# Performance work log

Hardware: AMD Instinct MI355X
Metric: run time of the kernel (lower is better)

## Reference

```python
import jax, jax.numpy as jnp
import numpy as np

B, Nq, C = 1, 40000, 256
Hh, L, P = 8, 4, 8
hd = C // Hh
LEVEL_SHAPES = [(128, 128), (64, 64), (32, 32), (16, 16)]


def setup_inputs() -> dict:
    key = jax.random.key(0)
    ks = jax.random.split(key, 16)
    inp = {}
    inp['query'] = jax.random.normal(ks[0], (B, Nq, C), jnp.float32)
    # reference points in [-1, 1] normalized coords (x, y)
    inp['reference_points'] = jax.random.uniform(ks[1], (B, Nq, L, 2), jnp.float32) * 2.0 - 1.0
    for i, (h, w) in enumerate(LEVEL_SHAPES):
        inp[f'feat{i}'] = jax.random.normal(ks[2 + i], (B, C, h, w), jnp.float32)
    # learned params (torch Linear y = x @ W + b, W stored as [in, out])
    inp['W_off'] = jax.random.normal(ks[6], (C, Hh * L * P * 2), jnp.float32) * 0.02
    inp['b_off'] = jax.random.normal(ks[7], (Hh * L * P * 2,), jnp.float32) * 0.5
    inp['W_attn'] = jax.random.normal(ks[8], (C, Hh * L * P), jnp.float32) * 0.02
    inp['b_attn'] = jnp.zeros((Hh * L * P,), jnp.float32)
    inp['W_val'] = jax.random.normal(ks[9], (C, C), jnp.float32) * (1.0 / np.sqrt(C))
    inp['b_val'] = jnp.zeros((C,), jnp.float32)
    inp['W_out'] = jax.random.normal(ks[10], (C, C), jnp.float32) * (1.0 / np.sqrt(C))
    inp['b_out'] = jnp.zeros((C,), jnp.float32)
    return inp


def _deform_sample(v, coords):
    # Bilinear grid_sample, align_corners=True, zeros padding.
    # v: [B, Hh, H, W, hd]; coords: [B, Hh, S, 2] in [-1, 1] (x, y)
    _, _, H, W, _ = v.shape
    x = (coords[..., 0] + 1.0) * 0.5 * (W - 1)
    y = (coords[..., 1] + 1.0) * 0.5 * (H - 1)
    x0 = jnp.floor(x)
    y0 = jnp.floor(y)
    vflat = v.reshape(v.shape[0], v.shape[1], H * W, v.shape[4])

    def corner(xi, yi, w):
        inb = (xi >= 0) & (xi <= W - 1) & (yi >= 0) & (yi <= H - 1)
        idx = (jnp.clip(yi, 0, H - 1) * W + jnp.clip(xi, 0, W - 1)).astype(jnp.int32)
        g = jnp.take_along_axis(vflat, idx[..., None], axis=2)  # [B,Hh,S,hd]
        return g * (w * inb)[..., None]

    return (corner(x0, y0, (x0 + 1 - x) * (y0 + 1 - y))
            + corner(x0 + 1, y0, (x - x0) * (y0 + 1 - y))
            + corner(x0, y0 + 1, (x0 + 1 - x) * (y - y0))
            + corner(x0 + 1, y0 + 1, (x - x0) * (y - y0)))


def reference(query, feat0, feat1, feat2, feat3, reference_points,
              W_off, b_off, W_attn, b_attn, W_val, b_val, W_out, b_out):
    feats = [feat0, feat1, feat2, feat3]
    off = (query @ W_off + b_off).reshape(B, Nq, Hh, L, P, 2)
    w = (query @ W_attn + b_attn).reshape(B, Nq, Hh, L, P)
    w = jax.nn.softmax(w, axis=-1)  # softmax over points, per level
    # samp: [B, Nq, Hh, L, P, 2]
    samp = reference_points[:, :, None, :, None, :] + jnp.tanh(off) * 0.25

    out = jnp.zeros((B, Nq, Hh, hd), jnp.float32)
    for l, f in enumerate(feats):
        Hl, Wl = f.shape[2], f.shape[3]
        v = jnp.einsum('bchw,cd->bhwd', f, W_val) + b_val  # value proj
        v = v.reshape(B, Hl, Wl, Hh, hd).transpose(0, 3, 1, 2, 4)  # [B,Hh,H,W,hd]
        coords = samp[:, :, :, l].transpose(0, 2, 1, 3, 4).reshape(B, Hh, Nq * P, 2)
        s = _deform_sample(v, coords).reshape(B, Hh, Nq, P, hd)
        wl = w[:, :, :, l].transpose(0, 2, 1, 3)  # [B,Hh,Nq,P]
        out = out + jnp.einsum('bhnpd,bhnp->bnhd', s, wl)

    return out.reshape(B, Nq, C) @ W_out + b_out
```

## Files before the change

### kernel.cpp

```cpp
#include <hip/hip_runtime.h>
#include <hip/hip_fp16.h>
#include <math.h>

#define NQ 40000

typedef short s16x8 __attribute__((ext_vector_type(8)));
typedef float f32x4 __attribute__((ext_vector_type(4)));

static constexpr int HLa[4] = {128, 64, 32, 16};
static constexpr int HWa[4] = {16384, 4096, 1024, 256};
static constexpr int VB[4] = {0, 4194304, 5242880, 5505024};

__device__ __forceinline__ short bf16hi(float x) {
    union { float f; unsigned u; } v; v.f = x;
    unsigned r = v.u + 0x7FFFu + ((v.u >> 16) & 1u);
    return (short)(r >> 16);
}
__device__ __forceinline__ float bf16f(short s) {
    union { unsigned u; float f; } v; v.u = ((unsigned)(unsigned short)s) << 16;
    return v.f;
}
__device__ __forceinline__ float fast_tanh(float x) {
    float xc = fminf(fmaxf(x, -15.f), 15.f);
    float e = __expf(2.f * xc);
    return (e - 1.f) / (e + 1.f);
}
#define MFMA16(a, b, c) __builtin_amdgcn_mfma_f32_16x16x32_bf16(a, b, c, 0, 0, 0)

__global__ __launch_bounds__(256) void prep_w(
    const float* __restrict__ Woff, const float* __restrict__ Wattn,
    const float* __restrict__ Wout, short* __restrict__ WtH, short* __restrict__ WtL)
{
    int r = blockIdx.x, c = threadIdx.x;
    float x;
    if (r < 512)      x = Woff[c * 512 + r];
    else if (r < 768) x = Wattn[c * 256 + (r - 512)];
    else              x = Wout[c * 256 + (r - 768)];
    short hi = bf16hi(x);
    WtH[r * 256 + c] = hi;
    WtL[r * 256 + c] = bf16hi(x - bf16f(hi));
}

__global__ __launch_bounds__(256) void vproj_kernel(
    const float* __restrict__ f0, const float* __restrict__ f1,
    const float* __restrict__ f2, const float* __restrict__ f3,
    const float* __restrict__ Wv, const float* __restrict__ bv,
    __half* __restrict__ v)
{
    __shared__ float fT[256 * 16];

    int bid = blockIdx.x;
    const float* f;
    int base, HWl, hw0;
    if (bid < 1024)      { f = f0; base = VB[0]; HWl = 16384; hw0 = bid * 16; }
    else if (bid < 1280) { f = f1; base = VB[1]; HWl = 4096;  hw0 = (bid - 1024) * 16; }
    else if (bid < 1344) { f = f2; base = VB[2]; HWl = 1024;  hw0 = (bid - 1280) * 16; }
    else                 { f = f3; base = VB[3]; HWl = 256;   hw0 = (bid - 1344) * 16; }

    int t = threadIdx.x;
    for (int k = 0; k < 16; ++k) {
        int idx = k * 256 + t;
        int c = idx >> 4, j = idx & 15;
        fT[idx] = f[c * HWl + hw0 + j];
    }
    __syncthreads();

    int to4 = (t & 63) * 4;
    int hw4 = (t >> 6) * 4;

    float4 bv4 = *(const float4*)(bv + to4);
    float acc[4][4];
    #pragma unroll
    for (int i = 0; i < 4; ++i) {
        acc[i][0] = bv4.x; acc[i][1] = bv4.y; acc[i][2] = bv4.z; acc[i][3] = bv4.w;
    }

    #pragma unroll 4
    for (int c = 0; c < 256; ++c) {
        float4 w4 = *(const float4*)(Wv + c * 256 + to4);
        float4 fv = *(const float4*)(fT + c * 16 + hw4);
        float fa[4] = {fv.x, fv.y, fv.z, fv.w};
        float wa[4] = {w4.x, w4.y, w4.z, w4.w};
        #pragma unroll
        for (int i = 0; i < 4; ++i)
            #pragma unroll
            for (int j = 0; j < 4; ++j)
                acc[i][j] += fa[i] * wa[j];
    }

    int hh = to4 >> 5, dd4 = to4 & 31;
    #pragma unroll
    for (int i = 0; i < 4; ++i) {
        int hw = hw0 + hw4 + i;
        __half2 h0 = __floats2half2_rn(acc[i][0], acc[i][1]);
        __half2 h1 = __floats2half2_rn(acc[i][2], acc[i][3]);
        uint2 st = make_uint2(*(unsigned*)&h0, *(unsigned*)&h1);
        *(uint2*)(v + base + (hh * HWl + hw) * 32 + dd4) = st;
    }
}

__global__ __launch_bounds__(256, 4) void msda_kernel(
    const float* __restrict__ query, const float* __restrict__ refp,
    const float* __restrict__ boff,  const float* __restrict__ battn,
    const float* __restrict__ bout,
    const short* __restrict__ WtH,   const short* __restrict__ WtL,
    const __half* __restrict__ v,    float* __restrict__ out)
{
    __shared__ __align__(16) char lds[37888];
    short*    sQh  = (short*)lds;
    short*    sQl  = (short*)(lds + 8448);
    float*    offL = (float*)lds;
    uint2*    sPWh = (uint2*)(lds + 8448);
    float*    sWf  = (float*)(lds + 16896);
    unsigned* sPI  = (unsigned*)(lds + 33280);
    float*    sR   = (float*)(lds + 37376);

    const int t = threadIdx.x;
    const int n0 = blockIdx.x * 16;
    const int wv = t >> 6, lane = t & 63;
    const int mrow = lane & 15, kg = lane >> 4;

    for (int k2 = 0; k2 < 16; ++k2) {
        float x = query[(n0 + k2) * 256 + t];
        short hi = bf16hi(x);
        sQh[k2 * 264 + t] = hi;
        sQl[k2 * 264 + t] = bf16hi(x - bf16f(hi));
    }
    if (t < 128) sR[t] = refp[n0 * 8 + t];
    __syncthreads();

    f32x4 accO[8], accA[4];
    {
        f32x4 z = {0.f, 0.f, 0.f, 0.f};
        #pragma unroll
        for (int j = 0; j < 8; ++j) accO[j] = z;
        #pragma unroll
        for (int j = 0; j < 4; ++j) accA[j] = z;
    }
    {
        const short* offH = WtH + (wv * 128 + mrow) * 256 + kg * 8;
        const short* offLo = WtL + (wv * 128 + mrow) * 256 + kg * 8;
        const short* attH = WtH + (512 + wv * 64 + mrow) * 256 + kg * 8;
        const short* attL = WtL + (512 + wv * 64 + mrow) * 256 + kg * 8;
        const int aoff = mrow * 264 + kg * 8;
        #pragma unroll
        for (int kk = 0; kk < 8; ++kk) {
            s16x8 ah = *(const s16x8*)(sQh + aoff + kk * 32);
            s16x8 al = *(const s16x8*)(sQl + aoff + kk * 32);
            #pragma unroll
            for (int j = 0; j < 8; ++j) {
                s16x8 bh = *(const s16x8*)(offH + j * 4096 + kk * 32);
                s16x8 bl = *(const s16x8*)(offLo + j * 4096 + kk * 32);
                accO[j] = MFMA16(ah, bh, accO[j]);
                accO[j] = MFMA16(al, bh, accO[j]);
                accO[j] = MFMA16(ah, bl, accO[j]);
            }
            #pragma unroll
            for (int ja = 0; ja < 4; ++ja) {
                s16x8 bh = *(const s16x8*)(attH + ja * 4096 + kk * 32);
                s16x8 bl = *(const s16x8*)(attL + ja * 4096 + kk * 32);
                accA[ja] = MFMA16(ah, bh, accA[ja]);
                accA[ja] = MFMA16(al, bh, accA[ja]);
                accA[ja] = MFMA16(ah, bl, accA[ja]);
            }
        }
    }
    #pragma unroll
    for (int j = 0; j < 8; ++j) {
        float bb = boff[wv * 128 + j * 16 + mrow];
        #pragma unroll
        for (int r = 0; r < 4; ++r) accO[j][r] += bb;
    }
    #pragma unroll
    for (int ja = 0; ja < 4; ++ja) {
        float bb = battn[wv * 64 + ja * 16 + mrow];
        #pragma unroll
        for (int r = 0; r < 4; ++r) accA[ja][r] += bb;
    }

    #pragma unroll
    for (int ja = 0; ja < 4; ++ja) {
        int hh = 2 * wv + (ja >> 1);
        int l  = ((ja & 1) << 1) | (mrow >> 3);
        int p  = mrow & 7;
        #pragma unroll
        for (int r = 0; r < 4; ++r) {
            float x = accA[ja][r];
            float m = fmaxf(x, __shfl_xor(x, 1));
            m = fmaxf(m, __shfl_xor(m, 2));
            m = fmaxf(m, __shfl_xor(m, 4));
            float e = __expf(x - m);
            float s = e + __shfl_xor(e, 1);
            s += __shfl_xor(s, 2);
            s += __shfl_xor(s, 4);
            int q = kg * 4 + r;
            sWf[q * 256 + hh * 32 + l * 8 + p] = e / s;
        }
    }
    __syncthreads();

    const int dd2 = t & 15, hhpS = (t >> 4) & 1, qp = t >> 5;

    for (int k = 0; k < 4; ++k) {
        if (wv == k) {
            #pragma unroll
            for (int j = 0; j < 8; ++j)
                #pragma unroll
                for (int r = 0; r < 4; ++r)
                    offL[(kg * 4 + r) * 132 + j * 16 + mrow] = accO[j][r];
        }
        __syncthreads();

        #pragma unroll
        for (int it = 0; it < 4; ++it) {
            int s = it * 256 + t;
            int q = s >> 6, hhL = (s >> 5) & 1, l = (s >> 3) & 3, p = s & 7;
            const int Wl = 128 >> l;
            const float scl = 0.5f * (float)(Wl - 1);
            float lx = offL[q * 132 + hhL * 64 + l * 16 + p * 2];
            float ly = offL[q * 132 + hhL * 64 + l * 16 + p * 2 + 1];
            float w  = sWf[q * 256 + (2 * k + hhL) * 32 + l * 8 + p];
            float rx = sR[q * 8 + l * 2], ry = sR[q * 8 + l * 2 + 1];
            float cx = rx + fast_tanh(lx) * 0.25f;
            float cy = ry + fast_tanh(ly) * 0.25f;
            float xx = (cx + 1.f) * scl, yy = (cy + 1.f) * scl;
            float x0f = floorf(xx), y0f = floorf(yy);
            float fx = xx - x0f, fy = yy - y0f;
            int x0 = (int)x0f, y0 = (int)y0f;
            int xc0 = min(max(x0, 0), Wl - 1);
            int xc1 = min(max(x0 + 1, 0), Wl - 1);
            int yc0 = min(max(y0, 0), Wl - 1);
            int yc1 = min(max(y0 + 1, 0), Wl - 1);
            bool bx0 = (x0 >= 0) & (x0 < Wl);
            bool bx1 = (x0 + 1 >= 0) & (x0 + 1 < Wl);
            bool by0 = (y0 >= 0) & (y0 < Wl);
            bool by1 = (y0 + 1 >= 0) & (y0 + 1 < Wl);
            float w00 = (bx0 && by0) ? (1.f - fx) * (1.f - fy) * w : 0.f;
            float w01 = (bx1 && by0) ? fx * (1.f - fy) * w : 0.f;
            float w10 = (bx0 && by1) ? (1.f - fx) * fy * w : 0.f;
            float w11 = (bx1 && by1) ? fx * fy * w : 0.f;
            unsigned pw = (unsigned)(yc0 * Wl + xc0)
                        | ((unsigned)(xc1 - xc0) << 14)
                        | ((unsigned)(yc1 - yc0) << 15);
            sPI[s] = pw;
            __half2 hA = __floats2half2_rn(w00, w01);
            __half2 hB = __floats2half2_rn(w10, w11);
            sPWh[s] = make_uint2(*(unsigned*)&hA, *(unsigned*)&hB);
        }
        __syncthreads();

        {
            const int hh = 2 * k + hhpS;
            #pragma unroll
            for (int qi2 = 0; qi2 < 2; ++qi2) {
                int qi = qp * 2 + qi2;
                float accx = 0.f, accy = 0.f;
                #pragma unroll
                for (int l = 0; l < 4; ++l) {
                    const int Wl = HLa[l];
                    const __half2* vl = (const __half2*)(v + VB[l] + hh * HWa[l] * 32 + dd2 * 2);
                    int sbase = ((qi * 2 + hhpS) * 4 + l) * 8;
                    #pragma unroll
                    for (int p = 0; p < 8; ++p) {
                        unsigned pw = sPI[sbase + p];
                        uint2 ww = sPWh[sbase + p];
                        float2 fa = __half22float2(*(__half2*)&ww.x);
                        float2 fb = __half22float2(*(__half2*)&ww.y);
                        int idx = pw & 0x3FFF;
                        int dxo = ((pw >> 14) & 1) * 16;
                        int dyo = ((pw >> 15) & 1) * (Wl * 16);
                        const __half2* b00 = vl + idx * 16;
                        float2 f00 = __half22float2(b00[0]);
                        float2 f01 = __half22float2(b00[dxo]);
                        float2 f10 = __half22float2(b00[dyo]);
                        float2 f11 = __half22float2(b00[dxo + dyo]);
                        accx += fa.x * f00.x + fa.y * f01.x + fb.x * f10.x + fb.y * f11.x;
                        accy += fa.x * f00.y + fa.y * f01.y + fb.x * f10.y + fb.y * f11.y;
                    }
                }
                *(float2*)(sWf + qi * 256 + hh * 32 + dd2 * 2) = make_float2(accx, accy);
            }
        }
        __syncthreads();
    }

    {
        int q = t >> 4, c0 = (t & 15) * 16;
        #pragma unroll
        for (int j = 0; j < 16; ++j) {
            float x = sWf[q * 256 + c0 + j];
            short hi = bf16hi(x);
            sQh[q * 264 + c0 + j] = hi;
            sQl[q * 264 + c0 + j] = bf16hi(x - bf16f(hi));
        }
    }
    __syncthreads();

    {
        f32x4 accE[4];
        f32x4 z = {0.f, 0.f, 0.f, 0.f};
        #pragma unroll
        for (int e = 0; e < 4; ++e) accE[e] = z;
        const short* outH = WtH + (768 + wv * 64 + mrow) * 256 + kg * 8;
        const short* outL = WtL + (768 + wv * 64 + mrow) * 256 + kg * 8;
        const int aoff = mrow * 264 + kg * 8;
        #pragma unroll
        for (int kk = 0; kk < 8; ++kk) {
            s16x8 ah = *(const s16x8*)(sQh + aoff + kk * 32);
            s16x8 al = *(const s16x8*)(sQl + aoff + kk * 32);
            #pragma unroll
            for (int e = 0; e < 4; ++e) {
                s16x8 bh = *(const s16x8*)(outH + e * 4096 + kk * 32);
                s16x8 bl = *(const s16x8*)(outL + e * 4096 + kk * 32);
                accE[e] = MFMA16(ah, bh, accE[e]);
                accE[e] = MFMA16(al, bh, accE[e]);
                accE[e] = MFMA16(ah, bl, accE[e]);
            }
        }
        #pragma unroll
        for (int e = 0; e < 4; ++e) {
            int col = wv * 64 + e * 16 + mrow;
            float bb = bout[col];
            #pragma unroll
            for (int r = 0; r < 4; ++r)
                out[(n0 + kg * 4 + r) * 256 + col] = accE[e][r] + bb;
        }
    }
}

extern "C" void kernel_launch(void* const* d_in, const int* in_sizes, int n_in,
                              void* d_out, int out_size, void* d_ws, size_t ws_size,
                              hipStream_t stream) {
    const float* query = (const float*)d_in[0];
    const float* refp  = (const float*)d_in[1];
    const float* f0    = (const float*)d_in[2];
    const float* f1    = (const float*)d_in[3];
    const float* f2    = (const float*)d_in[4];
    const float* f3    = (const float*)d_in[5];
    const float* Woff  = (const float*)d_in[6];
    const float* boff  = (const float*)d_in[7];
    const float* Wattn = (const float*)d_in[8];
    const float* battn = (const float*)d_in[9];
    const float* Wval  = (const float*)d_in[10];
    const float* bval  = (const float*)d_in[11];
    const float* Wout  = (const float*)d_in[12];
    const float* bout  = (const float*)d_in[13];

    __half* v  = (__half*)d_ws;
    short* WtH = (short*)((char*)d_ws + 11141120);
    short* WtL = WtH + 262144;
    float* outp = (float*)d_out;

    prep_w<<<1024, 256, 0, stream>>>(Woff, Wattn, Wout, WtH, WtL);
    vproj_kernel<<<1360, 256, 0, stream>>>(f0, f1, f2, f3, Wval, bval, v);
    msda_kernel<<<2500, 256, 0, stream>>>(query, refp, boff, battn, bout,
                                          WtH, WtL, v, outp);
}
```

Measured before the change: 540.8 us.

## Shrink LDS with fp16 buffers, use packed half2 FMA for bilinear gather

The fp32 softmax-weight/output staging buffer becomes an fp16 buffer, which cuts LDS per block so launch bounds can target 5 blocks per CU. The sampling loop is reorganised so each thread handles 4 channels of one query and head and loads 8-byte chunks per corner. The corner blends are done with packed half2 FMAs before accumulating in fp32. This adds fp16 rounding to the attention weights, the per-point blend and the intermediate output, which may cost accuracy, in exchange for fewer instructions and higher occupancy.

```diff
diff --git a/kernel.cpp b/kernel.cpp
--- a/kernel.cpp
+++ b/kernel.cpp
@@ -99,21 +99,21 @@
     }
 }
 
-__global__ __launch_bounds__(256, 4) void msda_kernel(
+__global__ __launch_bounds__(256, 5) void msda_kernel(
     const float* __restrict__ query, const float* __restrict__ refp,
     const float* __restrict__ boff,  const float* __restrict__ battn,
     const float* __restrict__ bout,
     const short* __restrict__ WtH,   const short* __restrict__ WtL,
     const __half* __restrict__ v,    float* __restrict__ out)
 {
-    __shared__ __align__(16) char lds[37888];
+    __shared__ __align__(16) char lds[29952];
     short*    sQh  = (short*)lds;
     short*    sQl  = (short*)(lds + 8448);
     float*    offL = (float*)lds;
     uint2*    sPWh = (uint2*)(lds + 8448);
-    float*    sWf  = (float*)(lds + 16896);
-    unsigned* sPI  = (unsigned*)(lds + 33280);
-    float*    sR   = (float*)(lds + 37376);
+    __half*   sWh  = (__half*)(lds + 16896);
+    unsigned* sPI  = (unsigned*)(lds + 25344);
+    float*    sR   = (float*)(lds + 29440);
 
     const int t = threadIdx.x;
     const int n0 = blockIdx.x * 16;
@@ -194,12 +194,14 @@
             s += __shfl_xor(s, 2);
             s += __shfl_xor(s, 4);
             int q = kg * 4 + r;
-            sWf[q * 256 + hh * 32 + l * 8 + p] = e / s;
+            sWh[q * 264 + hh * 32 + l * 8 + p] = __float2half_rn(e / s);
         }
     }
     __syncthreads();
 
-    const int dd2 = t & 15, hhpS = (t >> 4) & 1, qp = t >> 5;
+    const int clS  = t & 7;
+    const int hhLS = (t >> 3) & 1;
+    const int qS   = t >> 4;
 
     for (int k = 0; k < 4; ++k) {
         if (wv == k) {
@@ -219,7 +221,7 @@
             const float scl = 0.5f * (float)(Wl - 1);
             float lx = offL[q * 132 + hhL * 64 + l * 16 + p * 2];
             float ly = offL[q * 132 + hhL * 64 + l * 16 + p * 2 + 1];
-            float w  = sWf[q * 256 + (2 * k + hhL) * 32 + l * 8 + p];
+            float w  = __half2float(sWh[q * 264 + (2 * k + hhL) * 32 + l * 8 + p]);
             float rx = sR[q * 8 + l * 2], ry = sR[q * 8 + l * 2 + 1];
             float cx = rx + fast_tanh(lx) * 0.25f;
             float cy = ry + fast_tanh(ly) * 0.25f;
@@ -250,48 +252,63 @@
         __syncthreads();
 
         {
-            const int hh = 2 * k + hhpS;
-            #pragma unroll
-            for (int qi2 = 0; qi2 < 2; ++qi2) {
-                int qi = qp * 2 + qi2;
-                float accx = 0.f, accy = 0.f;
+            const int hh = 2 * k + hhLS;
+            float ac0 = 0.f, ac1 = 0.f, ac2 = 0.f, ac3 = 0.f;
+            #pragma unroll
+            for (int l = 0; l < 4; ++l) {
+                const int Wl = HLa[l];
+                const __half2* vl = (const __half2*)(v + VB[l] + hh * HWa[l] * 32 + clS * 4);
+                const int sbase = qS * 64 + hhLS * 32 + l * 8;
                 #pragma unroll
-                for (int l = 0; l < 4; ++l) {
-                    const int Wl = HLa[l];
-                    const __half2* vl = (const __half2*)(v + VB[l] + hh * HWa[l] * 32 + dd2 * 2);
-                    int sbase = ((qi * 2 + hhpS) * 4 + l) * 8;
-                    #pragma unroll
-                    for (int p = 0; p < 8; ++p) {
-                        unsigned pw = sPI[sbase + p];
-                        uint2 ww = sPWh[sbase + p];
-                        float2 fa = __half22float2(*(__half2*)&ww.x);
-                        float2 fb = __half22float2(*(__half2*)&ww.y);
-                        int idx = pw & 0x3FFF;
-                        int dxo = ((pw >> 14) & 1) * 16;
-                        int dyo = ((pw >> 15) & 1) * (Wl * 16);
-                        const __half2* b00 = vl + idx * 16;
-                        float2 f00 = __half22float2(b00[0]);
-                        float2 f01 = __half22float2(b00[dxo]);
-                        float2 f10 = __half22float2(b00[dyo]);
-                        float2 f11 = __half22float2(b00[dxo + dyo]);
-                        accx += fa.x * f00.x + fa.y * f01.x + fb.x * f10.x + fb.y * f11.x;
-                        accy += fa.x * f00.y + fa.y * f01.y + fb.x * f10.y + fb.y * f11.y;
-                    }
+                for (int p = 0; p < 8; ++p) {
+                    unsigned pw = sPI[sbase + p];
+                    uint2 ww = sPWh[sbase + p];
+                    int idx = pw & 0x3FFF;
+                    int dxo = ((pw >> 14) & 1) * 16;
+                    int dyo = ((pw >> 15) & 1) * (Wl * 16);
+                    const __half2* b00 = vl + idx * 16;
+                    uint2 g00 = *(const uint2*)(b00);
+                    uint2 g01 = *(const uint2*)(b00 + dxo);
+                    uint2 g10 = *(const uint2*)(b00 + dyo);
+                    uint2 g11 = *(const uint2*)(b00 + dxo + dyo);
+                    __half2 wA = *(__half2*)&ww.x;
+                    __half2 wB = *(__half2*)&ww.y;
+                    __half2 w00 = __low2half2(wA),  w01 = __high2half2(wA);
+                    __half2 w10 = __low2half2(wB),  w11 = __high2half2(wB);
+                    __half2 s0 = __hmul2(w00, *(__half2*)&g00.x);
+                    s0 = __hfma2(w01, *(__half2*)&g01.x, s0);
+                    s0 = __hfma2(w10, *(__half2*)&g10.x, s0);
+                    s0 = __hfma2(w11, *(__half2*)&g11.x, s0);
+                    __half2 s1 = __hmul2(w00, *(__half2*)&g00.y);
+                    s1 = __hfma2(w01, *(__half2*)&g01.y, s1);
+                    s1 = __hfma2(w10, *(__half2*)&g10.y, s1);
+                    s1 = __hfma2(w11, *(__half2*)&g11.y, s1);
+                    float2 f0 = __half22float2(s0);
+                    float2 f1 = __half22float2(s1);
+                    ac0 += f0.x; ac1 += f0.y; ac2 += f1.x; ac3 += f1.y;
                 }
-                *(float2*)(sWf + qi * 256 + hh * 32 + dd2 * 2) = make_float2(accx, accy);
             }
+            __half2 o0 = __floats2half2_rn(ac0, ac1);
+            __half2 o1 = __floats2half2_rn(ac2, ac3);
+            *(uint2*)(sWh + qS * 264 + hh * 32 + clS * 4) =
+                make_uint2(*(unsigned*)&o0, *(unsigned*)&o1);
         }
         __syncthreads();
     }
 
     {
-        int q = t >> 4, c0 = (t & 15) * 16;
-        #pragma unroll
-        for (int j = 0; j < 16; ++j) {
-            float x = sWf[q * 256 + c0 + j];
-            short hi = bf16hi(x);
-            sQh[q * 264 + c0 + j] = hi;
-            sQl[q * 264 + c0 + j] = bf16hi(x - bf16f(hi));
+        int q = t & 15, seg = t >> 4;
+        const __half2* src = (const __half2*)(sWh + q * 264 + seg * 16);
+        short* dh = sQh + q * 264 + seg * 16;
+        short* dl = sQl + q * 264 + seg * 16;
+        #pragma unroll
+        for (int jj = 0; jj < 8; ++jj) {
+            float2 f = __half22float2(src[jj]);
+            short h0 = bf16hi(f.x), h1 = bf16hi(f.y);
+            dh[2 * jj]     = h0;
+            dh[2 * jj + 1] = h1;
+            dl[2 * jj]     = bf16hi(f.x - bf16f(h0));
+            dl[2 * jj + 1] = bf16hi(f.y - bf16f(h1));
         }
     }
     __syncthreads();
```

Measured after the change: 563.0 us. 4.1% more time.
